# Kernel tuning notes

Measured on AMD Instinct MI355X. Metric: run time of the kernel, lower is better.

The kernel has to match this reference:

```python
import jax, jax.numpy as jnp
import numpy as np

SQRT3 = 3.0 ** 0.5


def _mlp(emb, w1, w2):
    # e3nn FullyConnectedNet: no bias, weights ~ N(0,1), scaled by 1/sqrt(fan_in)
    h = jax.nn.relu(emb @ w1 / jnp.sqrt(jnp.float32(w1.shape[0])))
    return h @ w2 / jnp.sqrt(jnp.float32(w2.shape[0]))


def setup_inputs() -> dict:
    key = jax.random.key(0)
    ks = jax.random.split(key, 10)
    N, E = 10000, 160000
    x = jax.random.normal(ks[0], (N, 32), jnp.float32)          # 8x0e + 8x1o per node
    edge_src = jax.random.randint(ks[1], (E,), 0, N)
    edge_dst = jax.random.randint(ks[2], (E,), 0, N)
    edge_vec = jax.random.normal(ks[3], (E, 3), jnp.float32)
    emb = jax.random.uniform(ks[4], (E, 10), jnp.float32)       # radial basis embedding
    norm = jax.random.uniform(ks[5], (E,), jnp.float32)
    fc1_w1 = jax.random.normal(ks[6], (10, 16), jnp.float32)
    fc1_w2 = jax.random.normal(ks[7], (16, 512), jnp.float32)   # tp.weight_numel = 512
    fc2_w1 = jax.random.normal(ks[8], (10, 16), jnp.float32)
    fc2_w2 = jax.random.normal(ks[9], (16, 384), jnp.float32)   # tp2.weight_numel = 384
    return dict(x=x, edge_src=edge_src, edge_dst=edge_dst, edge_vec=edge_vec,
                emb=emb, norm=norm, num_nodes=N,
                fc1_w1=fc1_w1, fc1_w2=fc1_w2, fc2_w1=fc2_w1, fc2_w2=fc2_w2)


def reference(x, edge_src, edge_dst, edge_vec, emb, norm, num_nodes,
              fc1_w1, fc1_w2, fc2_w1, fc2_w2):
    E = edge_vec.shape[0]
    # spherical harmonics lmax=1, normalize=True, 'component' norm: Y0=1, Y1=sqrt(3)*r_hat
    r = edge_vec / jnp.linalg.norm(edge_vec, axis=1, keepdims=True)
    sh1 = SQRT3 * r                                     # [E,3]; sh0 == 1

    # gather + concat -> in1 irreps (8x0e+8x1o)+(8x0e+8x1o) ~ 16 scalars, 16 vectors
    xs, xd = x[edge_src], x[edge_dst]
    s1 = jnp.concatenate([xs[:, :8], xd[:, :8]], axis=1)                       # [E,16]
    v1 = jnp.concatenate([xs[:, 8:].reshape(E, 8, 3),
                          xd[:, 8:].reshape(E, 8, 3)], axis=1)                 # [E,16,3]

    # --- TP1: per-edge weights from radial MLP, paths ss->s, vv->s, sv->v, vs->v ---
    w = _mlp(emb, fc1_w1, fc1_w2)                       # [E,512]
    Wss = w[:, 0:128].reshape(E, 16, 8)
    Wvv = w[:, 128:256].reshape(E, 16, 8)
    Wsv = w[:, 256:384].reshape(E, 16, 8)
    Wvs = w[:, 384:512].reshape(E, 16, 8)
    a1 = 1.0 / jnp.sqrt(32.0)                           # path normalization, fan_in=16+16
    vdot1 = jnp.einsum('euk,ek->eu', v1, sh1) / SQRT3   # CG 1o x 1o -> 0e
    s_t = a1 * (jnp.einsum('eu,euw->ew', s1, Wss) + jnp.einsum('eu,euw->ew', vdot1, Wvv))
    v_t = a1 * (jnp.einsum('eu,euw->ew', s1, Wsv)[:, :, None] * sh1[:, None, :]
                + jnp.einsum('euk,euw->ewk', v1, Wvs))  # [E,8,3]

    # --- TP2 into gate irreps: 8x0e scalars + 8x0e gates + 8x1o gated ---
    w2 = _mlp(emb, fc2_w1, fc2_w2)                      # [E,384]
    Ass = w2[:, 0:64].reshape(E, 8, 8);   Avv = w2[:, 64:128].reshape(E, 8, 8)
    Bss = w2[:, 128:192].reshape(E, 8, 8); Bvv = w2[:, 192:256].reshape(E, 8, 8)
    Csv = w2[:, 256:320].reshape(E, 8, 8); Cvs = w2[:, 320:384].reshape(E, 8, 8)
    a2 = 1.0 / jnp.sqrt(16.0)                           # fan_in=8+8 per output group
    vdot2 = jnp.einsum('euk,ek->eu', v_t, sh1) / SQRT3
    scal = a2 * (jnp.einsum('eu,euw->ew', s_t, Ass) + jnp.einsum('eu,euw->ew', vdot2, Avv))
    gates = a2 * (jnp.einsum('eu,euw->ew', s_t, Bss) + jnp.einsum('eu,euw->ew', vdot2, Bvv))
    vecs = a2 * (jnp.einsum('eu,euw->ew', s_t, Csv)[:, :, None] * sh1[:, None, :]
                 + jnp.einsum('euk,euw->ewk', v_t, Cvs))

    # --- gate (act=tanh on scalars and gates) + per-edge norm + scatter-sum ---
    edge_out = jnp.concatenate([jnp.tanh(scal),
                                (vecs * jnp.tanh(gates)[:, :, None]).reshape(E, 24)], axis=1)
    edge_out = edge_out * norm[:, None]                 # [E,32]
    return jax.ops.segment_sum(edge_out, edge_dst, num_segments=num_nodes)
```

## Files before the change

### kernel.cpp

```cpp
#include <hip/hip_runtime.h>


#define EPB    64
#define BLOCK  256
#define NNP    10240
#define SLOT   144
#define MAXDEG 128

#define SQRT3_F      1.7320508075688772f
#define INV_SQRT3_F  0.5773502691896258f
#define INV_SQRT10_F 0.31622776601683794f
#define A1_4         0.044194173824159216f
#define A2_4         0.0625f

typedef _Float16 f16;
typedef f16 f16x2 __attribute__((ext_vector_type(2)));
typedef f16 f16x4 __attribute__((ext_vector_type(4)));
typedef float f32x4v __attribute__((ext_vector_type(4)));

#if defined(__HIP_DEVICE_COMPILE__)
#  if __has_builtin(__builtin_amdgcn_mfma_f32_16x16x16f16)
#    define MFMA16(a, b, c) __builtin_amdgcn_mfma_f32_16x16x16f16((a), (b), (c), 0, 0, 0)
#  else
#    define MFMA16(a, b, c) __builtin_amdgcn_mfma_f32_16x16x16_f16((a), (b), (c), 0, 0, 0)
#  endif
#else
#  define MFMA16(a, b, c) (c)
#endif

#define BFLY(v) { v += __shfl_xor(v, 16); v += __shfl_xor(v, 32); }

__global__ void zero_f32(float* __restrict__ p, int n) {
    int i = blockIdx.x * blockDim.x + threadIdx.x;
    if (i < n) p[i] = 0.0f;
}

__global__ void prep_hist(const float* __restrict__ W2, const float* __restrict__ W4,
                          f16* __restrict__ W2s, f16* __restrict__ W4s,
                          const int* __restrict__ edst, int* __restrict__ counts,
                          int* __restrict__ rank, int E) {
    int gid = blockIdx.x * blockDim.x + threadIdx.x;
    if (gid < E) {
        rank[gid] = atomicAdd(&counts[edst[gid]], 1);
    } else if (gid < E + 8192) {
        int idx = gid - E;
        int r = idx >> 4, h = idx & 15;
        int j = r >> 6, p = (r >> 4) & 3, u = r & 15;
        int q = p * 128 + u * 8 + j;
        float sc = (p == 1) ? (A1_4 * INV_SQRT3_F) : A1_4;
        W2s[r * 16 + h] = (f16)(W2[h * 512 + q] * sc);
    } else if (gid < E + 16384) {
        int idx = gid - E - 8192;
        int r = idx >> 4, h = idx & 15;
        int j = r >> 6, p = (r >> 3) & 7, u = r & 7;
        if (p < 6) {
            int q = p * 64 + u * 8 + j;
            float sc = (p == 1 || p == 3) ? (A2_4 * INV_SQRT3_F) : A2_4;
            W4s[r * 16 + h] = (f16)(W4[h * 384 + q] * sc);
        } else {
            W4s[r * 16 + h] = (f16)0.0f;
        }
    }
}

__global__ void gather_out(const f16* __restrict__ eout, const int* __restrict__ counts,
                           float* __restrict__ out, int nn) {
    const int tid = threadIdx.x;
    const int n = blockIdx.x * 16 + (tid >> 4);
    const int t = tid & 15;
    if (n >= nn) return;
    const size_t beg = (size_t)n * MAXDEG;
    int cnt = counts[n];
    if (cnt > MAXDEG) cnt = MAXDEG;
    float ax0 = 0.0f, ay0 = 0.0f, ax1 = 0.0f, ay1 = 0.0f;
    int k = 0;
    for (; k + 1 < cnt; k += 2) {
        f16x2 v0 = *(const f16x2*)&eout[(beg + k) * 32 + 2 * t];
        f16x2 v1 = *(const f16x2*)&eout[(beg + k + 1) * 32 + 2 * t];
        ax0 += (float)v0[0]; ay0 += (float)v0[1];
        ax1 += (float)v1[0]; ay1 += (float)v1[1];
    }
    if (k < cnt) {
        f16x2 v0 = *(const f16x2*)&eout[(beg + k) * 32 + 2 * t];
        ax0 += (float)v0[0]; ay0 += (float)v0[1];
    }
    float2 o; o.x = ax0 + ax1; o.y = ay0 + ay1;
    *(float2*)&out[(size_t)n * 32 + 2 * t] = o;
}

static __device__ __forceinline__ float tanh_fast(float x) {
    x = fminf(fmaxf(x, -15.0f), 15.0f);
    float e = __expf(2.0f * x);
    return (e - 1.0f) * __builtin_amdgcn_rcpf(e + 1.0f);
}

template <int ATOMIC>
__global__ void __launch_bounds__(BLOCK, 5) eq_nlmp(
    const float* __restrict__ x,
    const int*   __restrict__ esrc,
    const int*   __restrict__ edst,
    const float* __restrict__ evec,
    const float* __restrict__ emb,
    const float* __restrict__ nrm,
    const float* __restrict__ W1,
    const float* __restrict__ W3,
    const f16*   __restrict__ W2s,
    const f16*   __restrict__ W4s,
    const int*   __restrict__ rank,
    void*        __restrict__ dst_buf,
    int E)
{
    __shared__ __align__(16) char sED[EPB * SLOT];
    __shared__ float sEM [EPB * 12];
    __shared__ float sSH [EPB * 4];
    __shared__ f16   sH1 [EPB * 16];
    __shared__ f16   sH2 [EPB * 16];
    __shared__ float sW1t[16 * 12];
    __shared__ float sW3t[16 * 12];
    __shared__ int   sPOS[EPB];
    __shared__ int   sDST[EPB];
    __shared__ float sNRM[EPB];

    const int tid = threadIdx.x;
    const int ge0 = blockIdx.x * EPB;
    const int nvalid = (E - ge0 < EPB) ? (E - ge0) : EPB;

    if (tid < 160) {
        const int row = tid >> 4, hid = tid & 15;
        sW1t[hid * 12 + row] = W1[tid];
        sW3t[hid * 12 + row] = W3[tid];
    }

    const int e = tid >> 2;
    const int c = tid & 3;
    {
        int ge = ge0 + e; if (ge >= E) ge = E - 1;
        const int src = esrc[ge];
        const int dst = edst[ge];
        const float4* xs4 = (const float4*)(x + (size_t)src * 32);
        const float4* xd4 = (const float4*)(x + (size_t)dst * 32);
        float4 A0 = xs4[c], A1 = xs4[c + 4], B0 = xd4[c], B1 = xd4[c + 4];
        const float* a0p = (const float*)&A0;
        const float* a1p = (const float*)&A1;
        const float* b0p = (const float*)&B0;
        const float* b1p = (const float*)&B1;
        f16* xph = (f16*)(sED + e * SLOT);
        #pragma unroll
        for (int m = 0; m < 4; ++m) {
            const int i = 4 * c + m;
            {
                int pos;
                if (i < 8) pos = 4 * i;
                else { int r = i - 8; int u = (r * 2731) >> 13; pos = 4 * u + 1 + (r - 3 * u); }
                xph[pos] = (f16)a0p[m];
            }
            {
                int r = i + 8; int u = (r * 2731) >> 13;
                xph[4 * u + 1 + (r - 3 * u)] = (f16)a1p[m];
            }
            {
                int pos;
                if (i < 8) pos = 32 + 4 * i;
                else { int r = i - 8; int u = (r * 2731) >> 13; pos = 32 + 4 * u + 1 + (r - 3 * u); }
                xph[pos] = (f16)b0p[m];
            }
            {
                int r = i + 8; int u = (r * 2731) >> 13;
                xph[32 + 4 * u + 1 + (r - 3 * u)] = (f16)b1p[m];
            }
        }
        float2 t = *(const float2*)(emb + (size_t)ge * 10 + 2 * c);
        sEM[e * 12 + 2 * c]     = t.x;
        sEM[e * 12 + 2 * c + 1] = t.y;
        if (c == 0) {
            float2 t2 = *(const float2*)(emb + (size_t)ge * 10 + 8);
            sEM[e * 12 + 8] = t2.x;
            sEM[e * 12 + 9] = t2.y;
        } else if (c == 1) {
            float vx = evec[(size_t)ge * 3 + 0];
            float vy = evec[(size_t)ge * 3 + 1];
            float vz = evec[(size_t)ge * 3 + 2];
            float rn = sqrtf(vx * vx + vy * vy + vz * vz);
            sSH[e * 4 + 0] = SQRT3_F * vx / rn;
            sSH[e * 4 + 1] = SQRT3_F * vy / rn;
            sSH[e * 4 + 2] = SQRT3_F * vz / rn;
            sSH[e * 4 + 3] = 0.0f;
        } else if (c == 2) {
            sNRM[e] = nrm[ge];
        } else {
            if (ATOMIC) sDST[e] = dst;
            else {
                int rk = rank[ge];
                if (rk > MAXDEG - 1) rk = MAXDEG - 1;
                sPOS[e] = dst * MAXDEG + rk;
            }
        }
    }
    __syncthreads();

    {
        float2 em0 = *(const float2*)&sEM[e * 12 + 0];
        float2 em1 = *(const float2*)&sEM[e * 12 + 2];
        float2 em2 = *(const float2*)&sEM[e * 12 + 4];
        float2 em3 = *(const float2*)&sEM[e * 12 + 6];
        float2 em4 = *(const float2*)&sEM[e * 12 + 8];
        #pragma unroll
        for (int k = 0; k < 4; ++k) {
            const int hid = c + 4 * k;
            {
                const float4 wa = *(const float4*)&sW1t[hid * 12 + 0];
                const float4 wb = *(const float4*)&sW1t[hid * 12 + 4];
                const float2 wc = *(const float2*)&sW1t[hid * 12 + 8];
                float acc = em0.x*wa.x + em0.y*wa.y + em1.x*wa.z + em1.y*wa.w
                          + em2.x*wb.x + em2.y*wb.y + em3.x*wb.z + em3.y*wb.w
                          + em4.x*wc.x + em4.y*wc.y;
                sH1[e * 16 + hid] = (f16)fmaxf(acc * INV_SQRT10_F, 0.0f);
            }
            {
                const float4 wa = *(const float4*)&sW3t[hid * 12 + 0];
                const float4 wb = *(const float4*)&sW3t[hid * 12 + 4];
                const float2 wc = *(const float2*)&sW3t[hid * 12 + 8];
                float acc = em0.x*wa.x + em0.y*wa.y + em1.x*wa.z + em1.y*wa.w
                          + em2.x*wb.x + em2.y*wb.y + em3.x*wb.z + em3.y*wb.w
                          + em4.x*wc.x + em4.y*wc.y;
                sH2[e * 16 + hid] = (f16)fmaxf(acc * INV_SQRT10_F, 0.0f);
            }
        }
    }

    const int l   = tid & 63;
    const int m16 = l & 15;
    const int g4  = (l >> 4) << 2;
    const int qid = l >> 4;
    const int le  = ((tid >> 6) << 4) + m16;

    const float4 shv = *(const float4*)&sSH[le * 4];
    const float  nnv = sNRM[le];

    float4 d[4]; float vd[4];
    #pragma unroll
    for (int r = 0; r < 4; ++r) {
        f16x4 t = *(const f16x4*)((const f16*)(sED + le * SLOT) + 4 * (g4 + r));
        d[r].x = (float)t[0]; d[r].y = (float)t[1];
        d[r].z = (float)t[2]; d[r].w = (float)t[3];
        vd[r] = d[r].y * shv.x + d[r].z * shv.y + d[r].w * shv.z;
    }
    const f16x4 bf = *(const f16x4*)&sH1[le * 16 + g4];
    const f16* __restrict__ w2l = W2s + m16 * 16 + g4;
    const f32x4v zz = (f32x4v){0.0f, 0.0f, 0.0f, 0.0f};
    float* __restrict__ stvt = (float*)(sED + le * SLOT);

    #pragma unroll
    for (int jb = 0; jb < 8; jb += 4) {
        float p0[4], p1[4], p2[4], p3[4];
        #pragma unroll
        for (int jo = 0; jo < 4; ++jo) {
            const int j = jb + jo;
            float sts, svs, vt0, vt1, vt2;
            {
                f16x4 af = *(const f16x4*)(w2l + (4 * j + 0) * 256);
                f32x4v a = MFMA16(af, bf, zz);
                sts = d[0].x*a[0] + d[1].x*a[1] + d[2].x*a[2] + d[3].x*a[3];
            }
            {
                f16x4 af = *(const f16x4*)(w2l + (4 * j + 1) * 256);
                f32x4v a = MFMA16(af, bf, zz);
                sts += vd[0]*a[0] + vd[1]*a[1] + vd[2]*a[2] + vd[3]*a[3];
            }
            {
                f16x4 af = *(const f16x4*)(w2l + (4 * j + 2) * 256);
                f32x4v a = MFMA16(af, bf, zz);
                svs = d[0].x*a[0] + d[1].x*a[1] + d[2].x*a[2] + d[3].x*a[3];
            }
            {
                f16x4 af = *(const f16x4*)(w2l + (4 * j + 3) * 256);
                f32x4v a = MFMA16(af, bf, zz);
                vt0 = d[0].y*a[0] + d[1].y*a[1] + d[2].y*a[2] + d[3].y*a[3];
                vt1 = d[0].z*a[0] + d[1].z*a[1] + d[2].z*a[2] + d[3].z*a[3];
                vt2 = d[0].w*a[0] + d[1].w*a[1] + d[2].w*a[2] + d[3].w*a[3];
            }
            p0[jo] = sts;
            p1[jo] = svs * shv.x + vt0;
            p2[jo] = svs * shv.y + vt1;
            p3[jo] = svs * shv.z + vt2;
        }
        #pragma unroll
        for (int jo = 0; jo < 4; ++jo) {
            BFLY(p0[jo]) BFLY(p1[jo]) BFLY(p2[jo]) BFLY(p3[jo])
        }
        if (l < 16) {
            #pragma unroll
            for (int jo = 0; jo < 4; ++jo) {
                float4 o; o.x = p0[jo]; o.y = p1[jo]; o.z = p2[jo]; o.w = p3[jo];
                *(float4*)&stvt[4 * (jb + jo)] = o;
            }
        }
    }

    const int ub = g4 & 4;
    float fsel[4], c0[4], c1[4], c2[4];
    {
        const bool hi = (l >= 32);
        #pragma unroll
        for (int r = 0; r < 4; ++r) {
            float4 d2 = *(const float4*)&stvt[4 * (ub + r)];
            float v2 = d2.y * shv.x + d2.z * shv.y + d2.w * shv.z;
            fsel[r] = hi ? v2   : d2.x;
            c0[r]   = hi ? d2.y : d2.x * shv.x;
            c1[r]   = hi ? d2.z : d2.x * shv.y;
            c2[r]   = hi ? d2.w : d2.x * shv.z;
        }
    }
    const f16x4 bf2 = *(const f16x4*)&sH2[le * 16 + g4];
    const f16* __restrict__ w4l = W4s + m16 * 16 + g4;
    float outj[8];

    #pragma unroll
    for (int jb = 0; jb < 8; jb += 4) {
        float q0[4], q1[4], q2[4], q3[4], q4[4];
        #pragma unroll
        for (int jo = 0; jo < 4; ++jo) {
            const int j = jb + jo;
            {
                f16x4 af = *(const f16x4*)(w4l + (4 * j + 0) * 256);
                f32x4v a = MFMA16(af, bf2, zz);
                q0[jo] = fsel[0]*a[0] + fsel[1]*a[1] + fsel[2]*a[2] + fsel[3]*a[3];
            }
            {
                f16x4 af = *(const f16x4*)(w4l + (4 * j + 1) * 256);
                f32x4v a = MFMA16(af, bf2, zz);
                q1[jo] = fsel[0]*a[0] + fsel[1]*a[1] + fsel[2]*a[2] + fsel[3]*a[3];
            }
            {
                f16x4 af = *(const f16x4*)(w4l + (4 * j + 2) * 256);
                f32x4v a = MFMA16(af, bf2, zz);
                q2[jo] = c0[0]*a[0] + c0[1]*a[1] + c0[2]*a[2] + c0[3]*a[3];
                q3[jo] = c1[0]*a[0] + c1[1]*a[1] + c1[2]*a[2] + c1[3]*a[3];
                q4[jo] = c2[0]*a[0] + c2[1]*a[1] + c2[2]*a[2] + c2[3]*a[3];
            }
        }
        #pragma unroll
        for (int jo = 0; jo < 4; ++jo) {
            BFLY(q0[jo]) BFLY(q1[jo]) BFLY(q2[jo]) BFLY(q3[jo]) BFLY(q4[jo])
        }
        #pragma unroll
        for (int jo = 0; jo < 4; ++jo) {
            const float ts = tanh_fast(q0[jo]) * nnv;
            const float tg = tanh_fast(q1[jo]) * nnv;
            outj[jb + jo] = (qid == 0) ? ts
                          : (qid == 1) ? q2[jo] * tg
                          : (qid == 2) ? q3[jo] * tg
                                       : q4[jo] * tg;
        }
    }

    if (ATOMIC) {
        float* outp = (float*)dst_buf;
        if (le < nvalid) {
            float* ob = outp + (size_t)sDST[le] * 32;
            #pragma unroll
            for (int j = 0; j < 8; ++j) {
                const int col = (qid == 0) ? j : (8 + 3 * j + (qid - 1));
                atomicAdd(ob + col, outj[j]);
            }
        }
    } else {
        f16* eoutp = (f16*)dst_buf;
        #pragma unroll
        for (int j = 0; j < 8; ++j) {
            const int col = (qid == 0) ? j : (8 + 3 * j + (qid - 1));
            stvt[col] = outj[j];
        }
        __syncthreads();
        #pragma unroll
        for (int k = 0; k < 2; ++k) {
            const int idx = tid + k * 256;
            const int ee = idx >> 3, q8 = idx & 7;
            if (ee < nvalid) {
                float4 v = *(const float4*)((const float*)(sED + ee * SLOT) + 4 * q8);
                f16x4 h;
                h[0] = (f16)v.x; h[1] = (f16)v.y; h[2] = (f16)v.z; h[3] = (f16)v.w;
                *(f16x4*)&eoutp[(size_t)sPOS[ee] * 32 + 4 * q8] = h;
            }
        }
    }
}

extern "C" void kernel_launch(void* const* d_in, const int* in_sizes, int n_in,
                              void* d_out, int out_size, void* d_ws, size_t ws_size,
                              hipStream_t stream) {
    const float* x    = (const float*)d_in[0];
    const int*   esrc = (const int*)  d_in[1];
    const int*   edst = (const int*)  d_in[2];
    const float* evec = (const float*)d_in[3];
    const float* emb  = (const float*)d_in[4];
    const float* nrm  = (const float*)d_in[5];
    const float* W1   = (const float*)d_in[7];
    const float* W2   = (const float*)d_in[8];
    const float* W3   = (const float*)d_in[9];
    const float* W4   = (const float*)d_in[10];
    float* out = (float*)d_out;

    const int E  = in_sizes[1];
    const int NN = out_size / 32;
    const int nbatch = (E + EPB - 1) / EPB;

    size_t o_w2s   = 0;
    size_t o_w4s   = o_w2s + 512 * 16 * 2;
    size_t o_cnt   = o_w4s + 512 * 16 * 2;
    size_t o_rank  = o_cnt + (size_t)NNP * 4;
    size_t o_eout  = (o_rank + (size_t)E * 4 + 255) & ~(size_t)255;
    size_t need    = o_eout + (size_t)NNP * MAXDEG * 64;

    char* ws = (char*)d_ws;
    f16* W2s = (f16*)(ws + o_w2s);
    f16* W4s = (f16*)(ws + o_w4s);
    int* counts = (int*)(ws + o_cnt);
    int* rank   = (int*)(ws + o_rank);
    f16* eout   = (f16*)(ws + o_eout);

    const int ph_threads = E + 16384;

    if (NN <= NNP && ws_size >= need) {
        hipMemsetAsync(counts, 0, (size_t)NN * 4, stream);
        prep_hist<<<(ph_threads + 255) / 256, 256, 0, stream>>>(
            W2, W4, W2s, W4s, edst, counts, rank, E);
        eq_nlmp<0><<<nbatch, BLOCK, 0, stream>>>(x, esrc, edst, evec, emb, nrm,
                                                 W1, W3, W2s, W4s, rank,
                                                 (void*)eout, E);
        gather_out<<<(NN + 15) / 16, 256, 0, stream>>>(eout, counts, out, NN);
    } else {
        hipMemsetAsync(counts, 0, (size_t)NNP * 4, stream);
        zero_f32<<<(out_size + 255) / 256, 256, 0, stream>>>(out, out_size);
        prep_hist<<<(ph_threads + 255) / 256, 256, 0, stream>>>(
            W2, W4, W2s, W4s, edst, counts, rank, E);
        eq_nlmp<1><<<nbatch, BLOCK, 0, stream>>>(x, esrc, edst, evec, emb, nrm,
                                                 W1, W3, W2s, W4s, nullptr,
                                                 (void*)out, E);
    }
}
```

Baseline: 62.97 us.

## Fuse degree histogram into main kernel and widen gather loads

The per-edge slot assignment (atomicAdd on per-destination counters) moves from the prep kernel into the main edge kernel, removing the rank array and the E-thread histogram pass with its extra read and write. The weight-reformatting prep becomes a small standalone kernel. gather_out now uses 8 threads per node with 4-wide f16 loads and float4 stores, halving thread count per node. Atomics now contend within the main kernel and slot order becomes nondeterministic, so summation order may vary.

```diff
diff --git a/kernel.cpp b/kernel.cpp
--- a/kernel.cpp
+++ b/kernel.cpp
@@ -35,22 +35,17 @@
     if (i < n) p[i] = 0.0f;
 }
 
-__global__ void prep_hist(const float* __restrict__ W2, const float* __restrict__ W4,
-                          f16* __restrict__ W2s, f16* __restrict__ W4s,
-                          const int* __restrict__ edst, int* __restrict__ counts,
-                          int* __restrict__ rank, int E) {
+__global__ void prep_w(const float* __restrict__ W2, const float* __restrict__ W4,
+                       f16* __restrict__ W2s, f16* __restrict__ W4s) {
     int gid = blockIdx.x * blockDim.x + threadIdx.x;
-    if (gid < E) {
-        rank[gid] = atomicAdd(&counts[edst[gid]], 1);
-    } else if (gid < E + 8192) {
-        int idx = gid - E;
-        int r = idx >> 4, h = idx & 15;
+    if (gid < 8192) {
+        int r = gid >> 4, h = gid & 15;
         int j = r >> 6, p = (r >> 4) & 3, u = r & 15;
         int q = p * 128 + u * 8 + j;
         float sc = (p == 1) ? (A1_4 * INV_SQRT3_F) : A1_4;
         W2s[r * 16 + h] = (f16)(W2[h * 512 + q] * sc);
-    } else if (gid < E + 16384) {
-        int idx = gid - E - 8192;
+    } else if (gid < 16384) {
+        int idx = gid - 8192;
         int r = idx >> 4, h = idx & 15;
         int j = r >> 6, p = (r >> 3) & 7, u = r & 7;
         if (p < 6) {
@@ -66,26 +61,27 @@
 __global__ void gather_out(const f16* __restrict__ eout, const int* __restrict__ counts,
                            float* __restrict__ out, int nn) {
     const int tid = threadIdx.x;
-    const int n = blockIdx.x * 16 + (tid >> 4);
-    const int t = tid & 15;
+    const int n = blockIdx.x * 32 + (tid >> 3);
+    const int t = tid & 7;
     if (n >= nn) return;
     const size_t beg = (size_t)n * MAXDEG;
     int cnt = counts[n];
     if (cnt > MAXDEG) cnt = MAXDEG;
-    float ax0 = 0.0f, ay0 = 0.0f, ax1 = 0.0f, ay1 = 0.0f;
+    float a0 = 0.0f, a1 = 0.0f, a2 = 0.0f, a3 = 0.0f;
+    float b0 = 0.0f, b1 = 0.0f, b2 = 0.0f, b3 = 0.0f;
     int k = 0;
     for (; k + 1 < cnt; k += 2) {
-        f16x2 v0 = *(const f16x2*)&eout[(beg + k) * 32 + 2 * t];
-        f16x2 v1 = *(const f16x2*)&eout[(beg + k + 1) * 32 + 2 * t];
-        ax0 += (float)v0[0]; ay0 += (float)v0[1];
-        ax1 += (float)v1[0]; ay1 += (float)v1[1];
+        f16x4 v0 = *(const f16x4*)&eout[(beg + k) * 32 + 4 * t];
+        f16x4 v1 = *(const f16x4*)&eout[(beg + k + 1) * 32 + 4 * t];
+        a0 += (float)v0[0]; a1 += (float)v0[1]; a2 += (float)v0[2]; a3 += (float)v0[3];
+        b0 += (float)v1[0]; b1 += (float)v1[1]; b2 += (float)v1[2]; b3 += (float)v1[3];
     }
     if (k < cnt) {
-        f16x2 v0 = *(const f16x2*)&eout[(beg + k) * 32 + 2 * t];
-        ax0 += (float)v0[0]; ay0 += (float)v0[1];
-    }
-    float2 o; o.x = ax0 + ax1; o.y = ay0 + ay1;
-    *(float2*)&out[(size_t)n * 32 + 2 * t] = o;
+        f16x4 v0 = *(const f16x4*)&eout[(beg + k) * 32 + 4 * t];
+        a0 += (float)v0[0]; a1 += (float)v0[1]; a2 += (float)v0[2]; a3 += (float)v0[3];
+    }
+    float4 o; o.x = a0 + b0; o.y = a1 + b1; o.z = a2 + b2; o.w = a3 + b3;
+    *(float4*)&out[(size_t)n * 32 + 4 * t] = o;
 }
 
 static __device__ __forceinline__ float tanh_fast(float x) {
@@ -106,7 +102,7 @@
     const float* __restrict__ W3,
     const f16*   __restrict__ W2s,
     const f16*   __restrict__ W4s,
-    const int*   __restrict__ rank,
+    int*         __restrict__ counts,
     void*        __restrict__ dst_buf,
     int E)
 {
@@ -189,8 +185,8 @@
             sNRM[e] = nrm[ge];
         } else {
             if (ATOMIC) sDST[e] = dst;
-            else {
-                int rk = rank[ge];
+            else if (e < nvalid) {
+                int rk = atomicAdd(&counts[dst], 1);
                 if (rk > MAXDEG - 1) rk = MAXDEG - 1;
                 sPOS[e] = dst * MAXDEG + rk;
             }
@@ -408,32 +404,25 @@
     size_t o_w2s   = 0;
     size_t o_w4s   = o_w2s + 512 * 16 * 2;
     size_t o_cnt   = o_w4s + 512 * 16 * 2;
-    size_t o_rank  = o_cnt + (size_t)NNP * 4;
-    size_t o_eout  = (o_rank + (size_t)E * 4 + 255) & ~(size_t)255;
+    size_t o_eout  = (o_cnt + (size_t)NNP * 4 + 255) & ~(size_t)255;
     size_t need    = o_eout + (size_t)NNP * MAXDEG * 64;
 
     char* ws = (char*)d_ws;
     f16* W2s = (f16*)(ws + o_w2s);
     f16* W4s = (f16*)(ws + o_w4s);
     int* counts = (int*)(ws + o_cnt);
-    int* rank   = (int*)(ws + o_rank);
     f16* eout   = (f16*)(ws + o_eout);
 
-    const int ph_threads = E + 16384;
+    prep_w<<<64, 256, 0, stream>>>(W2, W4, W2s, W4s);
 
     if (NN <= NNP && ws_size >= need) {
         hipMemsetAsync(counts, 0, (size_t)NN * 4, stream);
-        prep_hist<<<(ph_threads + 255) / 256, 256, 0, stream>>>(
-            W2, W4, W2s, W4s, edst, counts, rank, E);
         eq_nlmp<0><<<nbatch, BLOCK, 0, stream>>>(x, esrc, edst, evec, emb, nrm,
-                                                 W1, W3, W2s, W4s, rank,
+                                                 W1, W3, W2s, W4s, counts,
                                                  (void*)eout, E);
-        gather_out<<<(NN + 15) / 16, 256, 0, stream>>>(eout, counts, out, NN);
+        gather_out<<<(NN + 31) / 32, 256, 0, stream>>>(eout, counts, out, NN);
     } else {
-        hipMemsetAsync(counts, 0, (size_t)NNP * 4, stream);
         zero_f32<<<(out_size + 255) / 256, 256, 0, stream>>>(out, out_size);
-        prep_hist<<<(ph_threads + 255) / 256, 256, 0, stream>>>(
-            W2, W4, W2s, W4s, edst, counts, rank, E);
         eq_nlmp<1><<<nbatch, BLOCK, 0, stream>>>(x, esrc, edst, evec, emb, nrm,
                                                  W1, W3, W2s, W4s, nullptr,
                                                  (void*)out, E);
```

New measurement: 58.86 us. 6.5% less time.
